# Kernel optimization log

Measured on AMD Instinct MI355X. Metric: run time of the kernel, lower is better.

Reference implementation:

```python
import jax, jax.numpy as jnp
import numpy as np

N_NODES = 100000


def _gcn_layer(x, W, b, src, dst, ew):
    # support = x @ W  (dense transform first, standard GCN)
    support = x @ W  # [N, out]
    # sparse propagate: out[i] = sum_{e: dst[e]=i} ew[e] * support[src[e]]
    msgs = support[src] * ew[:, None]  # [E, out]
    out = jax.ops.segment_sum(msgs, dst, num_segments=N_NODES)
    return out + b


def setup_inputs() -> dict:
    key = jax.random.key(0)
    ks = jax.random.split(key, 7)
    nfeat, nhid, nclass, E = 512, 256, 40, 3200000
    x = jax.random.normal(ks[0], (N_NODES, nfeat), dtype=jnp.float32)
    edge_index = jax.random.randint(ks[1], (2, E), 0, N_NODES, dtype=jnp.int32)
    edge_weight = jax.random.uniform(ks[2], (E,), dtype=jnp.float32)
    W1 = jax.random.normal(ks[3], (nfeat, nhid), dtype=jnp.float32) / np.sqrt(nfeat)
    b1 = jnp.zeros((nhid,), dtype=jnp.float32)
    W2 = jax.random.normal(ks[4], (nhid, nclass), dtype=jnp.float32) / np.sqrt(nhid)
    b2 = jnp.zeros((nclass,), dtype=jnp.float32)
    return {"x": x, "edge_index": edge_index, "edge_weight": edge_weight,
            "W1": W1, "b1": b1, "W2": W2, "b2": b2}


def reference(x, edge_index, edge_weight, W1, b1, W2, b2):
    src, dst = edge_index[0], edge_index[1]
    h = _gcn_layer(x, W1, b1, src, dst, edge_weight)
    h = jax.nn.relu(h)  # with_relu=True; dropout skipped (eval mode)
    h = _gcn_layer(h, W2, b2, src, dst, edge_weight)
    return jax.nn.log_softmax(h, axis=1)
```

## Files before the change

kernel.cpp:

```cpp
#include <hip/hip_runtime.h>
#include <math.h>

#define N_NODES 100000
#define M_PAD 100096
#define NFEAT 512
#define NHID 256
#define NCLASS 40
#define SUP2_LD 48

#define NBKT 250
#define NPB 400
#define BINA_CHUNK 3072
#define BCAP 14336

#define GEMM1_BLOCKS (M_PAD / 128)

typedef __attribute__((ext_vector_type(8))) short bf16x8;
typedef __attribute__((ext_vector_type(4))) float f32x4;

__device__ __forceinline__ unsigned short f2bf(float f) {
    unsigned int u = __builtin_bit_cast(unsigned int, f);
    u += 0x7fffu + ((u >> 16) & 1u);
    return (unsigned short)(u >> 16);
}
__device__ __forceinline__ void bf2x2(unsigned int u, float& f0, float& f1) {
    f0 = __builtin_bit_cast(float, u << 16);
    f1 = __builtin_bit_cast(float, u & 0xffff0000u);
}
__device__ __forceinline__ void gload16(const void* g, void* l) {
    __builtin_amdgcn_global_load_lds(
        (const __attribute__((address_space(1))) unsigned int*)g,
        (__attribute__((address_space(3))) unsigned int*)l, 16, 0, 0);
}
template <int CODE>
__device__ __forceinline__ float swzx(float v) {
    return __builtin_bit_cast(float,
        __builtin_amdgcn_ds_swizzle(__builtin_bit_cast(int, v), CODE));
}

#define CVTW_BLOCKS 512

__global__ __launch_bounds__(256) void k_init(int* __restrict__ bcur,
                                              const float* __restrict__ W1,
                                              unsigned short* __restrict__ w1t,
                                              const float* __restrict__ W2,
                                              uint4* __restrict__ w2f) {
    int b = blockIdx.x;
    int t = threadIdx.x;
    if (b == 0) {
        if (t < NBKT) bcur[t] = t * BCAP;
    } else if (b <= CVTW_BLOCKS) {
        int idx = (b - 1) * 256 + t;
        int n = idx >> 9, k = idx & 511;
        w1t[idx] = f2bf(W1[(size_t)k * NHID + n]);
    } else {
        for (int idx = t; idx < 8 * 3 * 64; idx += 256) {
            int ks = idx / 192;
            int rem = idx - ks * 192;
            int n = rem >> 6;
            int l = rem & 63;
            int col = n * 16 + (l & 15);
            int kbase = ks * 32 + (l >> 4) * 8;
            unsigned short o[8];
#pragma unroll
            for (int j = 0; j < 8; ++j)
                o[j] = (col < NCLASS) ? f2bf(W2[(size_t)(kbase + j) * NCLASS + col]) : 0;
            w2f[idx] = *(const uint4*)o;
        }
    }
}

__device__ __forceinline__ void binA_body(char* smbase, int t, int cblk,
                                          const int* __restrict__ src,
                                          const int* __restrict__ dst,
                                          const float* __restrict__ ew,
                                          int* __restrict__ bcur,
                                          uint2* __restrict__ tmp, int E) {
    uint2* sorted = (uint2*)smbase;
    unsigned char* bkt8 = (unsigned char*)(smbase + 24576);
    int* cnt = (int*)(smbase + 27648);
    int* startv = cnt + 256;
    int* offv = startv + 256;
    int* gb = offv + 256;
    int c0 = cblk * BINA_CHUNK;
    int n = min(BINA_CHUNK, E - c0);
    cnt[t] = 0;
    __syncthreads();
    for (int j = t; j < n; j += 256) {
        atomicAdd(&cnt[(unsigned)dst[c0 + j] / NPB], 1);
    }
    __syncthreads();
    int v = cnt[t];
    startv[t] = v;
    __syncthreads();
    for (int o = 1; o < 256; o <<= 1) {
        int a = (t >= o) ? startv[t - o] : 0;
        __syncthreads();
        startv[t] += a;
        __syncthreads();
    }
    int ex = startv[t] - v;
    __syncthreads();
    startv[t] = ex;
    offv[t] = ex;
    if (t < NBKT) gb[t] = (v > 0) ? atomicAdd(&bcur[t], v) : 0;
    __syncthreads();
    for (int j = t; j < n; j += 256) {
        int d = dst[c0 + j];
        int b = (unsigned)d / NPB;
        int dl = d - b * NPB;
        int r = atomicAdd(&offv[b], 1);
        sorted[r] = make_uint2((unsigned)src[c0 + j] | ((unsigned)dl << 17),
                               __builtin_bit_cast(unsigned, ew[c0 + j]));
        bkt8[r] = (unsigned char)b;
    }
    __syncthreads();
    for (int j = t; j < n; j += 256) {
        int b = bkt8[j];
        tmp[gb[b] + (j - startv[b])] = sorted[j];
    }
}

__device__ __forceinline__ void gemm1_body(char* smem, int t, int mb,
                                           const float* __restrict__ x,
                                           const unsigned short* __restrict__ w1t,
                                           unsigned short* __restrict__ sup1) {
    const int w = t >> 6, lane = t & 63;
    const int m0 = mb * 128;
    const int wm = w >> 1, wn = w & 1;
    const int r15 = lane & 15, hi = lane >> 4;

    f32x4 acc[4][8];
#pragma unroll
    for (int i = 0; i < 4; ++i)
#pragma unroll
        for (int j = 0; j < 8; ++j) acc[i][j] = (f32x4){0.f, 0.f, 0.f, 0.f};

    const char* wsrc = (const char*)w1t;

    float4 pa0, pa1, pa2, pa3;

#define A_LOAD(kt)                                                                     \
    {                                                                                  \
        int u0 = t, row0 = u0 >> 2, part0 = u0 & 3;                                    \
        int u1 = 256 + t, row1 = u1 >> 2, part1 = u1 & 3;                              \
        int gr0 = m0 + row0, gr1 = m0 + row1;                                          \
        if (gr0 < N_NODES) {                                                           \
            const float* sp = x + (size_t)gr0 * NFEAT + (kt) * 32 + part0 * 8;         \
            pa0 = *(const float4*)sp;                                                  \
            pa1 = *(const float4*)(sp + 4);                                            \
        } else {                                                                       \
            pa0 = pa1 = make_float4(0.f, 0.f, 0.f, 0.f);                               \
        }                                                                              \
        if (gr1 < N_NODES) {                                                           \
            const float* sp = x + (size_t)gr1 * NFEAT + (kt) * 32 + part1 * 8;         \
            pa2 = *(const float4*)sp;                                                  \
            pa3 = *(const float4*)(sp + 4);                                            \
        } else {                                                                       \
            pa2 = pa3 = make_float4(0.f, 0.f, 0.f, 0.f);                               \
        }                                                                              \
    }

#define A_STORE(b)                                                                     \
    {                                                                                  \
        char* Ab = smem + (b) * 8192;                                                  \
        int u0 = t, row0 = u0 >> 2, part0 = u0 & 3;                                    \
        int u1 = 256 + t, row1 = u1 >> 2, part1 = u1 & 3;                              \
        unsigned short ob[8];                                                          \
        ob[0] = f2bf(pa0.x); ob[1] = f2bf(pa0.y); ob[2] = f2bf(pa0.z);                 \
        ob[3] = f2bf(pa0.w); ob[4] = f2bf(pa1.x); ob[5] = f2bf(pa1.y);                 \
        ob[6] = f2bf(pa1.z); ob[7] = f2bf(pa1.w);                                      \
        *(uint4*)(Ab + row0 * 64 + ((part0 ^ ((row0 >> 1) & 3)) << 4)) =               \
            *(const uint4*)ob;                                                         \
        ob[0] = f2bf(pa2.x); ob[1] = f2bf(pa2.y); ob[2] = f2bf(pa2.z);                 \
        ob[3] = f2bf(pa2.w); ob[4] = f2bf(pa3.x); ob[5] = f2bf(pa3.y);                 \
        ob[6] = f2bf(pa3.z); ob[7] = f2bf(pa3.w);                                      \
        *(uint4*)(Ab + row1 * 64 + ((part1 ^ ((row1 >> 1) & 3)) << 4)) =               \
            *(const uint4*)ob;                                                         \
    }

#define B_STAGE(kt, b)                                                                 \
    {                                                                                  \
        char* Bb = smem + 16384 + (b) * 16384;                                         \
        _Pragma("unroll") for (int i = 0; i < 4; ++i) {                                \
            int u = i * 256 + t;                                                       \
            int nrow = u >> 2, part = u & 3;                                           \
            int q = part ^ ((nrow >> 1) & 3);                                          \
            gload16(wsrc + (size_t)nrow * 1024 + (kt) * 64 + q * 16, Bb + u * 16);     \
        }                                                                              \
    }

    A_LOAD(0);
    A_STORE(0);
    B_STAGE(0, 0);
    for (int kt = 0; kt < 16; ++kt) {
        __syncthreads();
        if (kt < 15) {
            A_LOAD(kt + 1);
            B_STAGE(kt + 1, (kt + 1) & 1);
        }
        const char* Ab = smem + (kt & 1) * 8192;
        const char* Bb = smem + 16384 + (kt & 1) * 16384;
        bf16x8 a[4], bb[8];
#pragma unroll
        for (int i = 0; i < 4; ++i) {
            int r = wm * 64 + i * 16 + r15;
            a[i] = *(const bf16x8*)(Ab + r * 64 + ((hi ^ ((r >> 1) & 3)) << 4));
        }
#pragma unroll
        for (int j = 0; j < 8; ++j) {
            int n = wn * 128 + j * 16 + r15;
            bb[j] = *(const bf16x8*)(Bb + n * 64 + ((hi ^ ((n >> 1) & 3)) << 4));
        }
#pragma unroll
        for (int i = 0; i < 4; ++i)
#pragma unroll
            for (int j = 0; j < 8; ++j)
                acc[i][j] = __builtin_amdgcn_mfma_f32_16x16x32_bf16(a[i], bb[j], acc[i][j], 0, 0, 0);
        if (kt < 15) A_STORE((kt + 1) & 1);
    }
#undef A_LOAD
#undef A_STORE
#undef B_STAGE

#pragma unroll
    for (int i = 0; i < 4; ++i) {
        int rowb = m0 + wm * 64 + i * 16 + hi * 4;
#pragma unroll
        for (int j = 0; j < 8; ++j) {
            int col = wn * 128 + j * 16 + r15;
#pragma unroll
            for (int r = 0; r < 4; ++r)
                sup1[(size_t)(rowb + r) * NHID + col] = f2bf(acc[i][j][r]);
        }
    }
}

__global__ __launch_bounds__(256) void k_fat(const float* __restrict__ x,
                                             const unsigned short* __restrict__ w1t,
                                             unsigned short* __restrict__ sup1,
                                             const int* __restrict__ src,
                                             const int* __restrict__ dst,
                                             const float* __restrict__ ew,
                                             int* __restrict__ bcur,
                                             uint2* __restrict__ tmp, int E) {
    __shared__ __align__(16) char smem[49152];
    int b = blockIdx.x;
    int t = threadIdx.x;
    if (b < GEMM1_BLOCKS) {
        gemm1_body(smem, t, b, x, w1t, sup1);
    } else {
        binA_body(smem, t, b - GEMM1_BLOCKS, src, dst, ew, bcur, tmp, E);
    }
}

__global__ __launch_bounds__(256) void k_binB(const uint2* __restrict__ tmp,
                                              const int* __restrict__ bcur,
                                              int* __restrict__ rowptr,
                                              uint2* __restrict__ cedge) {
    __shared__ int sc[256];
    __shared__ int nc[NPB];
    __shared__ int st[NPB];
    int b = blockIdx.x, t = threadIdx.x;
    int c = (t < NBKT) ? (bcur[t] - t * BCAP) : 0;
    sc[t] = c;
    __syncthreads();
    for (int o = 1; o < 256; o <<= 1) {
        int a = (t >= o) ? sc[t - o] : 0;
        __syncthreads();
        sc[t] += a;
        __syncthreads();
    }
    int base = (b == 0) ? 0 : sc[b - 1];
    int mycnt = sc[b] - base;
    int total = sc[NBKT - 1];
    __syncthreads();
    for (int i = t; i < NPB; i += 256) nc[i] = 0;
    __syncthreads();
    const uint2* srcp = tmp + (size_t)b * BCAP;
    for (int j = t; j < mycnt; j += 256) atomicAdd(&nc[srcp[j].x >> 17], 1);
    __syncthreads();
    int v0 = nc[t];
    sc[t] = v0;
    __syncthreads();
    for (int o = 1; o < 256; o <<= 1) {
        int a = (t >= o) ? sc[t - o] : 0;
        __syncthreads();
        sc[t] += a;
        __syncthreads();
    }
    int tot0 = sc[255];
    st[t] = sc[t] - v0;
    __syncthreads();
    int v1 = (t < NPB - 256) ? nc[256 + t] : 0;
    sc[t] = v1;
    __syncthreads();
    for (int o = 1; o < 256; o <<= 1) {
        int a = (t >= o) ? sc[t - o] : 0;
        __syncthreads();
        sc[t] += a;
        __syncthreads();
    }
    if (t < NPB - 256) st[256 + t] = tot0 + sc[t] - v1;
    __syncthreads();
    int n0 = b * NPB;
    for (int i = t; i < NPB; i += 256) {
        int s = base + st[i];
        rowptr[n0 + i] = s;
        st[i] = s;
    }
    if (b == NBKT - 1 && t == 0) rowptr[N_NODES] = total;
    __syncthreads();
    for (int j = t; j < mycnt; j += 256) {
        uint2 e = srcp[j];
        int dl = e.x >> 17;
        int addr = atomicAdd(&st[dl], 1);
        cedge[addr] = make_uint2(e.x & 0x1FFFFu, e.y);
    }
}

__global__ __launch_bounds__(256) void k_prop1(const unsigned short* __restrict__ sup1,
                                               const int* __restrict__ rowptr,
                                               const uint2* __restrict__ cedge,
                                               const float* __restrict__ b1,
                                               unsigned short* __restrict__ h1) {
    int gid = blockIdx.x * blockDim.x + threadIdx.x;
    int wid = gid >> 6;
    int lane = gid & 63;
    if (wid >= N_NODES) return;
    int beg = rowptr[wid], end = rowptr[wid + 1];
    float a0 = 0.f, a1 = 0.f, a2 = 0.f, a3 = 0.f;
    int e = beg;
    for (; e + 7 < end; e += 8) {
        uint2 ed[8];
#pragma unroll
        for (int q = 0; q < 8; ++q) ed[q] = cedge[e + q];
        uint2 r[8];
#pragma unroll
        for (int q = 0; q < 8; ++q)
            r[q] = *(const uint2*)(sup1 + (size_t)ed[q].x * NHID + lane * 4);
#pragma unroll
        for (int q = 0; q < 8; ++q) {
            float wq = __builtin_bit_cast(float, ed[q].y);
            float f0, f1, f2, f3;
            bf2x2(r[q].x, f0, f1);
            bf2x2(r[q].y, f2, f3);
            a0 += wq * f0; a1 += wq * f1; a2 += wq * f2; a3 += wq * f3;
        }
    }
    for (; e < end; ++e) {
        uint2 ed = cedge[e];
        float wq = __builtin_bit_cast(float, ed.y);
        uint2 rv = *(const uint2*)(sup1 + (size_t)ed.x * NHID + lane * 4);
        float f0, f1, f2, f3;
        bf2x2(rv.x, f0, f1);
        bf2x2(rv.y, f2, f3);
        a0 += wq * f0; a1 += wq * f1; a2 += wq * f2; a3 += wq * f3;
    }
    float4 bv = *(const float4*)(b1 + lane * 4);
    a0 = fmaxf(a0 + bv.x, 0.f);
    a1 = fmaxf(a1 + bv.y, 0.f);
    a2 = fmaxf(a2 + bv.z, 0.f);
    a3 = fmaxf(a3 + bv.w, 0.f);
    unsigned short o[4] = {f2bf(a0), f2bf(a1), f2bf(a2), f2bf(a3)};
    *(uint2*)(h1 + (size_t)wid * NHID + lane * 4) = *(const uint2*)o;
}

__global__ __launch_bounds__(256) void k_gemm2(const unsigned short* __restrict__ h1,
                                               const uint4* __restrict__ w2f,
                                               unsigned short* __restrict__ sup2) {
    int t = threadIdx.x;
    int w = t >> 6, lane = t & 63;
    int m0 = (blockIdx.x * 4 + w) * 16;
    int r15 = lane & 15, hi = lane >> 4;

    bf16x8 bfrag[8][3];
#pragma unroll
    for (int ks = 0; ks < 8; ++ks)
#pragma unroll
        for (int n = 0; n < 3; ++n)
            bfrag[ks][n] = __builtin_bit_cast(bf16x8, w2f[(ks * 3 + n) * 64 + lane]);

    f32x4 acc[3];
#pragma unroll
    for (int n = 0; n < 3; ++n) acc[n] = (f32x4){0.f, 0.f, 0.f, 0.f};

    const unsigned short* arow = h1 + (size_t)(m0 + r15) * NHID + hi * 8;
#pragma unroll
    for (int ks = 0; ks < 8; ++ks) {
        bf16x8 a = *(const bf16x8*)(arow + ks * 32);
#pragma unroll
        for (int n = 0; n < 3; ++n)
            acc[n] = __builtin_amdgcn_mfma_f32_16x16x32_bf16(a, bfrag[ks][n], acc[n], 0, 0, 0);
    }
#pragma unroll
    for (int n = 0; n < 3; ++n) {
        int col = n * 16 + r15;
#pragma unroll
        for (int r = 0; r < 4; ++r) {
            int row = m0 + hi * 4 + r;
            sup2[(size_t)row * SUP2_LD + col] = f2bf(acc[n][r]);
        }
    }
}

__global__ __launch_bounds__(256) void k_prop2(const unsigned short* __restrict__ sup2,
                                               const int* __restrict__ rowptr,
                                               const uint2* __restrict__ cedge,
                                               const float* __restrict__ b2,
                                               float* __restrict__ out) {
    int gid = blockIdx.x * blockDim.x + threadIdx.x;
    int wv = gid >> 6;
    int lane = gid & 63;
    int grp = lane >> 4;
    int gl = lane & 15;
    int wid = wv * 4 + grp;
    if (wid >= N_NODES) return;
    int beg = rowptr[wid], end = rowptr[wid + 1];
    bool act = gl < 10;
    int c4 = gl * 4;
    float acc0 = 0.f, acc1 = 0.f, acc2 = 0.f, acc3 = 0.f;
    int e = beg;
    for (; e + 7 < end; e += 8) {
        uint2 ed[8];
#pragma unroll
        for (int q = 0; q < 8; ++q) ed[q] = cedge[e + q];
        uint2 u[8];
#pragma unroll
        for (int q = 0; q < 8; ++q)
            u[q] = act ? *(const uint2*)(sup2 + (size_t)ed[q].x * SUP2_LD + c4)
                       : make_uint2(0u, 0u);
#pragma unroll
        for (int q = 0; q < 8; ++q) {
            float wq = __builtin_bit_cast(float, ed[q].y);
            float f0, f1, f2, f3;
            bf2x2(u[q].x, f0, f1);
            bf2x2(u[q].y, f2, f3);
            acc0 += wq * f0; acc1 += wq * f1; acc2 += wq * f2; acc3 += wq * f3;
        }
    }
    for (; e < end; ++e) {
        uint2 eq = cedge[e];
        uint2 u = act ? *(const uint2*)(sup2 + (size_t)eq.x * SUP2_LD + c4)
                      : make_uint2(0u, 0u);
        float wq = __builtin_bit_cast(float, eq.y);
        float f0, f1, f2, f3;
        bf2x2(u.x, f0, f1);
        bf2x2(u.y, f2, f3);
        acc0 += wq * f0; acc1 += wq * f1; acc2 += wq * f2; acc3 += wq * f3;
    }
    float v0 = -INFINITY, v1 = -INFINITY, v2 = -INFINITY, v3 = -INFINITY;
    if (act) {
        float4 bb = *(const float4*)(b2 + c4);
        v0 = acc0 + bb.x;
        v1 = acc1 + bb.y;
        v2 = acc2 + bb.z;
        v3 = acc3 + bb.w;
    }
    float m = fmaxf(fmaxf(v0, v1), fmaxf(v2, v3));
    m = fmaxf(m, swzx<0x201F>(m));
    m = fmaxf(m, swzx<0x101F>(m));
    m = fmaxf(m, swzx<0x081F>(m));
    m = fmaxf(m, swzx<0x041F>(m));
    float s = act ? (expf(v0 - m) + expf(v1 - m) + expf(v2 - m) + expf(v3 - m)) : 0.f;
    s += swzx<0x201F>(s);
    s += swzx<0x101F>(s);
    s += swzx<0x081F>(s);
    s += swzx<0x041F>(s);
    if (act) {
        float ls = logf(s);
        float4 o = make_float4(v0 - m - ls, v1 - m - ls, v2 - m - ls, v3 - m - ls);
        *(float4*)(out + (size_t)wid * NCLASS + c4) = o;
    }
}


extern "C" void kernel_launch(void* const* d_in, const int* in_sizes, int n_in,
                              void* d_out, int out_size, void* d_ws, size_t ws_size,
                              hipStream_t stream) {
    const float* x = (const float*)d_in[0];
    const int* ei = (const int*)d_in[1];
    const float* ew = (const float*)d_in[2];
    const float* W1 = (const float*)d_in[3];
    const float* b1 = (const float*)d_in[4];
    const float* W2 = (const float*)d_in[5];
    const float* b2 = (const float*)d_in[6];
    float* out = (float*)d_out;

    int E = in_sizes[1] / 2;
    const int* src = ei;
    const int* dst = ei + E;

    char* w = (char*)d_ws;
    size_t off = 0;
    auto alloc = [&](size_t bytes) {
        void* p = w + off;
        off += (bytes + 255) & ~(size_t)255;
        return p;
    };
    unsigned short* w1t = (unsigned short*)alloc((size_t)NHID * NFEAT * 2);
    unsigned short* sup1 = (unsigned short*)alloc((size_t)M_PAD * NHID * 2);
    unsigned short* h1 = (unsigned short*)alloc((size_t)M_PAD * NHID * 2);
    uint2* cedge = (uint2*)alloc((size_t)E * 8);
    uint2* tmp = (uint2*)alloc((size_t)NBKT * BCAP * 8);
    unsigned short* sup2 = (unsigned short*)alloc((size_t)M_PAD * SUP2_LD * 2);
    int* rowptr = (int*)alloc((size_t)(N_NODES + 1) * 4);
    int* bcur = (int*)alloc((size_t)NBKT * 4);
    uint4* w2f = (uint4*)alloc((size_t)8 * 3 * 64 * 16);

    const int BINA_BLOCKS = (E + BINA_CHUNK - 1) / BINA_CHUNK;

    k_init<<<1 + CVTW_BLOCKS + 1, 256, 0, stream>>>(bcur, W1, w1t, W2, w2f);
    k_fat<<<GEMM1_BLOCKS + BINA_BLOCKS, 256, 0, stream>>>(x, w1t, sup1,
                                                          src, dst, ew, bcur, tmp, E);
    k_binB<<<NBKT, 256, 0, stream>>>(tmp, bcur, rowptr, cedge);
    k_prop1<<<(N_NODES + 3) / 4, 256, 0, stream>>>(sup1, rowptr, cedge, b1, h1);
    k_gemm2<<<M_PAD / 64, 256, 0, stream>>>(h1, w2f, sup2);
    k_prop2<<<(N_NODES / 4 + 3) / 4, 256, 0, stream>>>(sup2, rowptr, cedge, b2, out);
}
```

Before: 478.5 us.

## Reschedule binning: overlap pass-B bucketing with GEMM1 and merge weight conversion into pass A

Binning pass A now runs in a pre-kernel together with the weight conversions, with the bucket counters zeroed by a memset. Pass B, the per-bucket CSR build, is merged into the fat kernel alongside the GEMM1 blocks. Bucket count drops to 200 with 500 nodes per bucket and a larger per-bucket capacity. The aim is to hide pass B behind the dense GEMM and remove one launch, at the cost of pass A no longer overlapping with GEMM1.

New measurement: 464.4 us (median of 2 runs). 2.9% less time.

```diff
diff --git a/kernel.cpp b/kernel.cpp
--- a/kernel.cpp
+++ b/kernel.cpp
@@ -8,10 +8,10 @@
 #define NCLASS 40
 #define SUP2_LD 48
 
-#define NBKT 250
-#define NPB 400
+#define NBKT 200
+#define NPB 500
 #define BINA_CHUNK 3072
-#define BCAP 14336
+#define BCAP 17920
 
 #define GEMM1_BLOCKS (M_PAD / 128)
 
@@ -36,38 +36,6 @@
 __device__ __forceinline__ float swzx(float v) {
     return __builtin_bit_cast(float,
         __builtin_amdgcn_ds_swizzle(__builtin_bit_cast(int, v), CODE));
-}
-
-#define CVTW_BLOCKS 512
-
-__global__ __launch_bounds__(256) void k_init(int* __restrict__ bcur,
-                                              const float* __restrict__ W1,
-                                              unsigned short* __restrict__ w1t,
-                                              const float* __restrict__ W2,
-                                              uint4* __restrict__ w2f) {
-    int b = blockIdx.x;
-    int t = threadIdx.x;
-    if (b == 0) {
-        if (t < NBKT) bcur[t] = t * BCAP;
-    } else if (b <= CVTW_BLOCKS) {
-        int idx = (b - 1) * 256 + t;
-        int n = idx >> 9, k = idx & 511;
-        w1t[idx] = f2bf(W1[(size_t)k * NHID + n]);
-    } else {
-        for (int idx = t; idx < 8 * 3 * 64; idx += 256) {
-            int ks = idx / 192;
-            int rem = idx - ks * 192;
-            int n = rem >> 6;
-            int l = rem & 63;
-            int col = n * 16 + (l & 15);
-            int kbase = ks * 32 + (l >> 4) * 8;
-            unsigned short o[8];
-#pragma unroll
-            for (int j = 0; j < 8; ++j)
-                o[j] = (col < NCLASS) ? f2bf(W2[(size_t)(kbase + j) * NCLASS + col]) : 0;
-            w2f[idx] = *(const uint4*)o;
-        }
-    }
 }
 
 __device__ __forceinline__ void binA_body(char* smbase, int t, int cblk,
@@ -117,7 +85,109 @@
     __syncthreads();
     for (int j = t; j < n; j += 256) {
         int b = bkt8[j];
-        tmp[gb[b] + (j - startv[b])] = sorted[j];
+        tmp[(size_t)b * BCAP + gb[b] + (j - startv[b])] = sorted[j];
+    }
+}
+
+#define CVTW_BLOCKS 512
+
+__global__ __launch_bounds__(256) void k_pre(const int* __restrict__ src,
+                                             const int* __restrict__ dst,
+                                             const float* __restrict__ ew,
+                                             int* __restrict__ bcur,
+                                             uint2* __restrict__ tmp, int E, int binaBlocks,
+                                             const float* __restrict__ W1,
+                                             unsigned short* __restrict__ w1t,
+                                             const float* __restrict__ W2,
+                                             uint4* __restrict__ w2f) {
+    __shared__ __align__(16) char smem[31744];
+    int b = blockIdx.x;
+    int t = threadIdx.x;
+    if (b < binaBlocks) {
+        binA_body(smem, t, b, src, dst, ew, bcur, tmp, E);
+    } else if (b < binaBlocks + CVTW_BLOCKS) {
+        int idx = (b - binaBlocks) * 256 + t;
+        int n = idx >> 9, k = idx & 511;
+        w1t[idx] = f2bf(W1[(size_t)k * NHID + n]);
+    } else {
+        for (int idx = t; idx < 8 * 3 * 64; idx += 256) {
+            int ks = idx / 192;
+            int rem = idx - ks * 192;
+            int n = rem >> 6;
+            int l = rem & 63;
+            int col = n * 16 + (l & 15);
+            int kbase = ks * 32 + (l >> 4) * 8;
+            unsigned short o[8];
+#pragma unroll
+            for (int j = 0; j < 8; ++j)
+                o[j] = (col < NCLASS) ? f2bf(W2[(size_t)(kbase + j) * NCLASS + col]) : 0;
+            w2f[idx] = *(const uint4*)o;
+        }
+    }
+}
+
+__device__ __forceinline__ void binB_body(char* smbase, int b, int t,
+                                          const uint2* __restrict__ tmp,
+                                          const int* __restrict__ bcur,
+                                          int* __restrict__ rowptr,
+                                          uint2* __restrict__ cedge) {
+    int* sc = (int*)smbase;
+    int* nc = sc + 256;
+    int* st = nc + NPB;
+    int c = (t < NBKT) ? bcur[t] : 0;
+    sc[t] = c;
+    __syncthreads();
+    for (int o = 1; o < 256; o <<= 1) {
+        int a = (t >= o) ? sc[t - o] : 0;
+        __syncthreads();
+        sc[t] += a;
+        __syncthreads();
+    }
+    int base = (b == 0) ? 0 : sc[b - 1];
+    int mycnt = sc[b] - base;
+    int total = sc[NBKT - 1];
+    __syncthreads();
+    for (int i = t; i < NPB; i += 256) nc[i] = 0;
+    __syncthreads();
+    const uint2* srcp = tmp + (size_t)b * BCAP;
+    for (int j = t; j < mycnt; j += 256) atomicAdd(&nc[srcp[j].x >> 17], 1);
+    __syncthreads();
+    int v0 = nc[t];
+    sc[t] = v0;
+    __syncthreads();
+    for (int o = 1; o < 256; o <<= 1) {
+        int a = (t >= o) ? sc[t - o] : 0;
+        __syncthreads();
+        sc[t] += a;
+        __syncthreads();
+    }
+    int tot0 = sc[255];
+    st[t] = sc[t] - v0;
+    __syncthreads();
+    int v1 = (t < NPB - 256) ? nc[256 + t] : 0;
+    sc[t] = v1;
+    __syncthreads();
+    for (int o = 1; o < 256; o <<= 1) {
+        int a = (t >= o) ? sc[t - o] : 0;
+        __syncthreads();
+        sc[t] += a;
+        __syncthreads();
+    }
+    if (t < NPB - 256) st[256 + t] = tot0 + sc[t] - v1;
+    __syncthreads();
+    int n0 = b * NPB;
+    for (int i = t; i < NPB; i += 256) {
+        int s = base + st[i];
+        rowptr[n0 + i] = s;
+        st[i] = s;
+    }
+    if (b == NBKT - 1 && t == 0) rowptr[N_NODES] = total;
+    __syncthreads();
+    for (int j = t; j < mycnt; j += 256) {
+        uint2 e = srcp[j];
+        int dl = e.x >> 17;
+        int addr = atomicAdd(&st[dl], 1);
+        cedge[addr] = make_uint2(e.x & 0x1FFFFu, e.y);
     }
 }
 
@@ -236,86 +306,20 @@
     }
 }
 
-__global__ __launch_bounds__(256) void k_fat(const float* __restrict__ x,
+__global__ __launch_bounds__(256) void k_fat(const uint2* __restrict__ tmp,
+                                             const int* __restrict__ bcur,
+                                             int* __restrict__ rowptr,
+                                             uint2* __restrict__ cedge,
+                                             const float* __restrict__ x,
                                              const unsigned short* __restrict__ w1t,
-                                             unsigned short* __restrict__ sup1,
-                                             const int* __restrict__ src,
-                                             const int* __restrict__ dst,
-                                             const float* __restrict__ ew,
-                                             int* __restrict__ bcur,
-                                             uint2* __restrict__ tmp, int E) {
+                                             unsigned short* __restrict__ sup1) {
     __shared__ __align__(16) char smem[49152];
     int b = blockIdx.x;
     int t = threadIdx.x;
-    if (b < GEMM1_BLOCKS) {
-        gemm1_body(smem, t, b, x, w1t, sup1);
+    if (b < NBKT) {
+        binB_body(smem, b, t, tmp, bcur, rowptr, cedge);
     } else {
-        binA_body(smem, t, b - GEMM1_BLOCKS, src, dst, ew, bcur, tmp, E);
-    }
-}
-
-__global__ __launch_bounds__(256) void k_binB(const uint2* __restrict__ tmp,
-                                              const int* __restrict__ bcur,
-                                              int* __restrict__ rowptr,
-                                              uint2* __restrict__ cedge) {
-    __shared__ int sc[256];
-    __shared__ int nc[NPB];
-    __shared__ int st[NPB];
-    int b = blockIdx.x, t = threadIdx.x;
-    int c = (t < NBKT) ? (bcur[t] - t * BCAP) : 0;
-    sc[t] = c;
-    __syncthreads();
-    for (int o = 1; o < 256; o <<= 1) {
-        int a = (t >= o) ? sc[t - o] : 0;
-        __syncthreads();
-        sc[t] += a;
-        __syncthreads();
-    }
-    int base = (b == 0) ? 0 : sc[b - 1];
-    int mycnt = sc[b] - base;
-    int total = sc[NBKT - 1];
-    __syncthreads();
-    for (int i = t; i < NPB; i += 256) nc[i] = 0;
-    __syncthreads();
-    const uint2* srcp = tmp + (size_t)b * BCAP;
-    for (int j = t; j < mycnt; j += 256) atomicAdd(&nc[srcp[j].x >> 17], 1);
-    __syncthreads();
-    int v0 = nc[t];
-    sc[t] = v0;
-    __syncthreads();
-    for (int o = 1; o < 256; o <<= 1) {
-        int a = (t >= o) ? sc[t - o] : 0;
-        __syncthreads();
-        sc[t] += a;
-        __syncthreads();
-    }
-    int tot0 = sc[255];
-    st[t] = sc[t] - v0;
-    __syncthreads();
-    int v1 = (t < NPB - 256) ? nc[256 + t] : 0;
-    sc[t] = v1;
-    __syncthreads();
-    for (int o = 1; o < 256; o <<= 1) {
-        int a = (t >= o) ? sc[t - o] : 0;
-        __syncthreads();
-        sc[t] += a;
-        __syncthreads();
-    }
-    if (t < NPB - 256) st[256 + t] = tot0 + sc[t] - v1;
-    __syncthreads();
-    int n0 = b * NPB;
-    for (int i = t; i < NPB; i += 256) {
-        int s = base + st[i];
-        rowptr[n0 + i] = s;
-        st[i] = s;
-    }
-    if (b == NBKT - 1 && t == 0) rowptr[N_NODES] = total;
-    __syncthreads();
-    for (int j = t; j < mycnt; j += 256) {
-        uint2 e = srcp[j];
-        int dl = e.x >> 17;
-        int addr = atomicAdd(&st[dl], 1);
-        cedge[addr] = make_uint2(e.x & 0x1FFFFu, e.y);
+        gemm1_body(smem, t, b - NBKT, x, w1t, sup1);
     }
 }
 
@@ -510,10 +514,10 @@
 
     const int BINA_BLOCKS = (E + BINA_CHUNK - 1) / BINA_CHUNK;
 
-    k_init<<<1 + CVTW_BLOCKS + 1, 256, 0, stream>>>(bcur, W1, w1t, W2, w2f);
-    k_fat<<<GEMM1_BLOCKS + BINA_BLOCKS, 256, 0, stream>>>(x, w1t, sup1,
-                                                          src, dst, ew, bcur, tmp, E);
-    k_binB<<<NBKT, 256, 0, stream>>>(tmp, bcur, rowptr, cedge);
+    hipMemsetAsync(bcur, 0, (size_t)NBKT * 4, stream);
+    k_pre<<<BINA_BLOCKS + CVTW_BLOCKS + 1, 256, 0, stream>>>(src, dst, ew, bcur, tmp, E,
+                                                             BINA_BLOCKS, W1, w1t, W2, w2f);
+    k_fat<<<NBKT + GEMM1_BLOCKS, 256, 0, stream>>>(tmp, bcur, rowptr, cedge, x, w1t, sup1);
     k_prop1<<<(N_NODES + 3) / 4, 256, 0, stream>>>(sup1, rowptr, cedge, b1, h1);
     k_gemm2<<<M_PAD / 64, 256, 0, stream>>>(h1, w2f, sup2);
     k_prop2<<<(N_NODES / 4 + 3) / 4, 256, 0, stream>>>(sup2, rowptr, cedge, b2, out);
```
